# Kernel optimization log

Hardware: AMD Instinct MI355X
Metric: run time of the kernel (lower is better)

## Reference

```python
import jax, jax.numpy as jnp
import numpy as np

B, T, IN, H = 1024, 128, 5, 100  # batch, seq_len, input_size, hidden_size


def setup_inputs() -> dict:
    key = jax.random.key(0)
    ks = jax.random.split(key, 20)
    bound = 1.0 / np.sqrt(H)  # PyTorch LSTM init: U(-1/sqrt(H), 1/sqrt(H))

    def u(k, shape):
        return jax.random.uniform(k, shape, jnp.float32, -bound, bound)

    inp = {"x": jax.random.normal(ks[0], (B, T, IN), jnp.float32)}
    i = 1
    for layer, din in [(0, IN), (1, 2 * H)]:
        for d in ("f", "b"):
            inp[f"w_ih_l{layer}{d}"] = u(ks[i], (4 * H, din)); i += 1
            inp[f"w_hh_l{layer}{d}"] = u(ks[i], (4 * H, H)); i += 1
            inp[f"b_ih_l{layer}{d}"] = u(ks[i], (4 * H,)); i += 1
            inp[f"b_hh_l{layer}{d}"] = u(ks[i], (4 * H,)); i += 1
    inp["fc_w"] = u(ks[17], (3, 2 * H))
    inp["fc_b"] = u(ks[18], (3,))
    return inp


def _run_dir(x, w_ih, w_hh, b_ih, b_hh, reverse):
    """One LSTM direction. x: [B,T,D] -> hidden seq [B,T,H]. PyTorch gate order i,f,g,o."""
    xT = jnp.swapaxes(x, 0, 1)  # [T,B,D]
    # precompute input contribution for all timesteps: [T,B,4H]
    xg = jnp.einsum('tbd,gd->tbg', xT, w_ih) + b_ih + b_hh

    def step(carry, g_in):
        h, c = carry
        g = g_in + h @ w_hh.T  # [B,4H]
        i, f, gg, o = jnp.split(g, 4, axis=-1)
        c = jax.nn.sigmoid(f) * c + jax.nn.sigmoid(i) * jnp.tanh(gg)
        h = jax.nn.sigmoid(o) * jnp.tanh(c)
        return (h, c), h

    b = x.shape[0]
    init = (jnp.zeros((b, H), x.dtype), jnp.zeros((b, H), x.dtype))
    _, hs = jax.lax.scan(step, init, xg, reverse=reverse)  # hs[t] aligned with time t
    return jnp.swapaxes(hs, 0, 1)  # [B,T,H]


def reference(x,
              w_ih_l0f, w_hh_l0f, b_ih_l0f, b_hh_l0f,
              w_ih_l0b, w_hh_l0b, b_ih_l0b, b_hh_l0b,
              w_ih_l1f, w_hh_l1f, b_ih_l1f, b_hh_l1f,
              w_ih_l1b, w_hh_l1b, b_ih_l1b, b_hh_l1b,
              fc_w, fc_b):
    # Layer 0 (bidirectional): [B,T,2H]
    h0 = jnp.concatenate([
        _run_dir(x, w_ih_l0f, w_hh_l0f, b_ih_l0f, b_hh_l0f, False),
        _run_dir(x, w_ih_l0b, w_hh_l0b, b_ih_l0b, b_hh_l0b, True),
    ], axis=-1)
    # (inter-layer dropout p=0.2 is identity in eval mode)
    # Layer 1 (bidirectional): [B,T,2H]
    h1 = jnp.concatenate([
        _run_dir(h0, w_ih_l1f, w_hh_l1f, b_ih_l1f, b_hh_l1f, False),
        _run_dir(h0, w_ih_l1b, w_hh_l1b, b_ih_l1b, b_hh_l1b, True),
    ], axis=-1)
    last = h1[:, -1, :]  # [B,2H]
    # (dropout p=0.5 is identity in eval mode)
    logits = last @ fc_w.T + fc_b  # [B,3]
    return jax.nn.softmax(logits, axis=1)
```

## Files before the change

### kernel.cpp

```cpp
#include <hip/hip_runtime.h>
#include <hip/hip_fp16.h>


typedef __attribute__((ext_vector_type(8))) short bf16x8;
typedef __attribute__((ext_vector_type(4))) float f32x4;

constexpr int Bsz = 1024, Tt = 128, IN_ = 5, H = 100, G = 400, D1 = 200;
constexpr int NP = 512;
constexpr int NT = 25;
constexpr int MB = 8;

__device__ __forceinline__ float sigm(float x)   { return 1.f / (1.f + __expf(-x)); }
__device__ __forceinline__ float tanhf_(float x) { return 1.f - 2.f / (__expf(2.f * x) + 1.f); }
__device__ __forceinline__ unsigned short f2bf(float f) {
  unsigned u = __float_as_uint(f);
  u += 0x7fff + ((u >> 16) & 1);
  return (unsigned short)(u >> 16);
}
__device__ __forceinline__ float partner8(float v) {
  return __uint_as_float(
      (unsigned)__builtin_amdgcn_ds_swizzle((int)__float_as_uint(v), 0x17));
}

__device__ __forceinline__ void pack_body(
    const float* wA, int KA, const float* wB, int KB, int kbo,
    const float* b1, const float* b2, int bias_k,
    unsigned short* dst, int Kg, int idx) {
  if (idx >= Kg * NP * 8) return;
  int jj = idx & 7, rest = idx >> 3;
  int np_ = rest % NP, g = rest / NP;
  int j = np_ >> 2, gate = np_ & 3;
  int k = g * 8 + jj;
  float v = 0.f;
  if (j < H) {
    int n = gate * H + j;
    if (k < KA) v = wA[n * KA + k];
    else if (KB > 0 && k >= kbo && k < kbo + KB) v = wB[n * KB + (k - kbo)];
    else if (k == bias_k) v = b1[n] + b2[n];
  }
  dst[idx] = f2bf(v);
}

__global__ void pack_all(
    const float* __restrict__ w_hh_l0f, const float* __restrict__ w_ih_l0f,
    const float* __restrict__ b_ih_l0f, const float* __restrict__ b_hh_l0f,
    const float* __restrict__ w_hh_l0b, const float* __restrict__ w_ih_l0b,
    const float* __restrict__ b_ih_l0b, const float* __restrict__ b_hh_l0b,
    const float* __restrict__ w_hh_l1f, const float* __restrict__ b_ih_l1f,
    const float* __restrict__ b_hh_l1f,
    const float* __restrict__ w_ih_l1f, const float* __restrict__ w_ih_l1b,
    const float* __restrict__ b_ih_l1b, const float* __restrict__ b_hh_l1b,
    unsigned short* __restrict__ pk0f, unsigned short* __restrict__ pk0b,
    unsigned short* __restrict__ pkhh, unsigned short* __restrict__ pkxg,
    unsigned short* __restrict__ pk1b) {
  int idx = blockIdx.x * 256 + threadIdx.x;
  switch (blockIdx.y) {
    case 0: pack_body(w_hh_l0f, 100, w_ih_l0f, 5, 100, b_ih_l0f, b_hh_l0f, 105, pk0f, 16, idx); break;
    case 1: pack_body(w_hh_l0b, 100, w_ih_l0b, 5, 100, b_ih_l0b, b_hh_l0b, 105, pk0b, 16, idx); break;
    case 2: pack_body(w_hh_l1f, 100, nullptr, 0, 0, b_ih_l1f, b_hh_l1f, -1, pkhh, 16, idx); break;
    case 3: pack_body(w_ih_l1f, 200, nullptr, 0, 0, b_ih_l1f, b_hh_l1f, 200, pkxg, 28, idx); break;
    default: pack_body(w_ih_l1b, 200, nullptr, 0, 0, b_ih_l1b, b_hh_l1b, 200, pk1b, 28, idx);
  }
}

__global__ __launch_bounds__(1024, 1) void lstm_l0(
    const float* __restrict__ x,
    const unsigned short* __restrict__ pk_f, const unsigned short* __restrict__ pk_b,
    unsigned short* __restrict__ h0fT, unsigned short* __restrict__ h0bT) {
  __shared__ __align__(16) short A_s[2][16][16][8];

  const int tid = threadIdx.x;
  const int lane = tid & 63, w = tid >> 6;
  const int q = lane >> 4, l16 = lane & 15;
  const int b0 = blockIdx.x * MB;
  const int dir = blockIdx.y;
  const unsigned short* pk = dir ? pk_b : pk_f;
  unsigned short* hT = dir ? h0bT : h0fT;

  for (int i = tid; i < 2 * 16 * 16 * 8; i += 1024) ((short*)A_s)[i] = 0;

  const int mtA = w, mtB = w + 16;
  const bool bvalid = (mtB < NT);
  bf16x8 wfA[4], wfB[4];
#pragma unroll
  for (int kt = 0; kt < 4; ++kt) {
    wfA[kt] = *(const bf16x8*)(pk + ((size_t)(kt * 4 + q) * NP + mtA * 16 + l16) * 8);
    wfB[kt] = *(const bf16x8*)(pk + ((size_t)(kt * 4 + q) * NP + mtB * 16 + l16) * 8);
  }
  float c = 0.f;
  const bool up = (l16 >= 8);
  const int mm = l16 & 7;
  const int j = (up ? mtB : mtA) * 4 + q;
  const bool valid = up ? bvalid : true;
  const int xm = tid / IN_, xe = tid - xm * IN_;
  const int sm = tid / 25, sj = (tid - (tid / 25) * 25) * 4;
  const float* xp = x + ((size_t)(b0 + xm) * Tt + (dir ? Tt - 2 : 1)) * IN_ + xe;
  const int xstride = dir ? -IN_ : IN_;
  unsigned short* hp =
      hT + ((size_t)(dir ? Tt - 1 : 0) * Bsz + b0 + sm) * H + sj;
  const int hstride = dir ? -(Bsz * H) : (Bsz * H);
  __syncthreads();
  if (tid < 16) {
    A_s[0][13][tid][1] = (short)f2bf(1.f);
    A_s[1][13][tid][1] = (short)f2bf(1.f);
  }
  if (tid < MB * IN_) {
    int t0 = dir ? (Tt - 1) : 0;
    int k = 100 + xe;
    A_s[0][k >> 3][xm][k & 7] =
        (short)f2bf(x[((size_t)(b0 + xm) * Tt + t0) * IN_ + xe]);
  }
  __syncthreads();

  int p = 0;
  for (int step = 0; step < Tt; ++step) {
    if (step > 0 && tid < 200) {
      uint2 hv = *(const uint2*)&A_s[p][sj >> 3][sm][sj & 7];
      *(uint2*)hp = hv;
      hp += hstride;
    }
    float xn = 0.f;
    const bool do_x = (tid < MB * IN_) && (step < Tt - 1);
    if (do_x) { xn = *xp; xp += xstride; }
    bf16x8 hfrag[4];
#pragma unroll
    for (int kt = 0; kt < 4; ++kt) hfrag[kt] = *(const bf16x8*)A_s[p][kt * 4 + q][l16];
    f32x4 accA = (f32x4){0.f, 0.f, 0.f, 0.f};
    f32x4 accB = (f32x4){0.f, 0.f, 0.f, 0.f};
#pragma unroll
    for (int kt = 0; kt < 4; ++kt)
      accA = __builtin_amdgcn_mfma_f32_16x16x32_bf16(wfA[kt], hfrag[kt], accA, 0, 0, 0);
    if (bvalid) {
#pragma unroll
      for (int kt = 0; kt < 4; ++kt)
        accB = __builtin_amdgcn_mfma_f32_16x16x32_bf16(wfB[kt], hfrag[kt], accB, 0, 0, 0);
    }
    float pb0 = partner8(accB[0]), pb1 = partner8(accB[1]);
    float pb2 = partner8(accB[2]), pb3 = partner8(accB[3]);
    float g0 = up ? pb0 : accA[0];
    float g1 = up ? pb1 : accA[1];
    float g2 = up ? pb2 : accA[2];
    float g3 = up ? pb3 : accA[3];
    float cc = sigm(g1) * c + sigm(g0) * tanhf_(g2);
    c = cc;
    float h = sigm(g3) * tanhf_(cc);
    if (valid) A_s[1 - p][j >> 3][mm][j & 7] = (short)f2bf(h);
    if (do_x) {
      int k = 100 + xe;
      A_s[1 - p][k >> 3][xm][k & 7] = (short)f2bf(xn);
    }
    __syncthreads();
    p ^= 1;
  }
  if (tid < 200) *(uint2*)hp = *(const uint2*)&A_s[p][sj >> 3][sm][sj & 7];
}

__global__ __launch_bounds__(1024, 1) void gemm_xg(
    const unsigned short* __restrict__ h0fT, const unsigned short* __restrict__ h0bT,
    const unsigned short* __restrict__ pkw, __half* __restrict__ xg) {
  __shared__ __align__(16) short B_s[28][64][8];
  const int tid = threadIdx.x;
  const int lane = tid & 63, w = tid >> 6;
  const int q = lane >> 4, l16 = lane & 15;
  const int r0 = blockIdx.x * 64;
  const size_t base = (size_t)r0 * H;

  for (int i = tid; i < 3 * 64 * 8; i += 1024) {
    int jj = i & 7, gl = i >> 9;
    ((short*)&B_s[25][0][0])[i] = (short)((gl == 0 && jj == 0) ? f2bf(1.f) : 0);
  }
  for (int idx = tid; idx < 1600; idx += 1024) {
    int m = idx / 25, j0 = (idx - (idx / 25) * 25) * 4;
    *(uint2*)&B_s[j0 >> 3][m][j0 & 7] = *(const uint2*)(h0fT + base + m * H + j0);
    int k = 100 + j0;
    *(uint2*)&B_s[k >> 3][m][k & 7] = *(const uint2*)(h0bT + base + m * H + j0);
  }

  const int mtA = w, mtB = w + 16;
  const bool bvalid = (mtB < NT);
  bf16x8 wfA[7], wfB[7];
#pragma unroll
  for (int kt = 0; kt < 7; ++kt) {
    wfA[kt] = *(const bf16x8*)(pkw + ((size_t)(kt * 4 + q) * NP + mtA * 16 + l16) * 8);
    wfB[kt] = *(const bf16x8*)(pkw + ((size_t)(kt * 4 + q) * NP + mtB * 16 + l16) * 8);
  }
  const int jA = mtA * 4 + q, jB = mtB * 4 + q;
  __syncthreads();

#pragma unroll
  for (int rg = 0; rg < 4; ++rg) {
    f32x4 accA = (f32x4){0.f, 0.f, 0.f, 0.f};
    f32x4 accB = (f32x4){0.f, 0.f, 0.f, 0.f};
#pragma unroll
    for (int kt = 0; kt < 7; ++kt) {
      bf16x8 hf = *(const bf16x8*)B_s[kt * 4 + q][rg * 16 + l16];
      accA = __builtin_amdgcn_mfma_f32_16x16x32_bf16(wfA[kt], hf, accA, 0, 0, 0);
      if (bvalid)
        accB = __builtin_amdgcn_mfma_f32_16x16x32_bf16(wfB[kt], hf, accB, 0, 0, 0);
    }
    const size_t row = (size_t)(r0 + rg * 16 + l16);
    {
      __half2 h01 = __floats2half2_rn(accA[0], accA[1]);
      __half2 h23 = __floats2half2_rn(accA[2], accA[3]);
      uint2 st; *(__half2*)&st.x = h01; *(__half2*)&st.y = h23;
      *(uint2*)(xg + row * G + 4 * jA) = st;
    }
    if (bvalid) {
      __half2 h01 = __floats2half2_rn(accB[0], accB[1]);
      __half2 h23 = __floats2half2_rn(accB[2], accB[3]);
      uint2 st; *(__half2*)&st.x = h01; *(__half2*)&st.y = h23;
      *(uint2*)(xg + row * G + 4 * jB) = st;
    }
  }
}

__global__ __launch_bounds__(1024, 1) void lstm_l1(
    const unsigned short* __restrict__ h0fT, const unsigned short* __restrict__ h0bT,
    const unsigned short* __restrict__ pk_hh, const unsigned short* __restrict__ pk1b,
    const __half* __restrict__ xg,
    const float* __restrict__ fc_w, const float* __restrict__ fc_b,
    float* __restrict__ out) {
  __shared__ __align__(16) short A_s[2][16][16][8];
  __shared__ __align__(16) short A2_s[28][16][8];
  __shared__ float hf_s[MB][H];
  __shared__ float hb_s[MB][H];
  __shared__ float fcw_s[3 * D1];
  __shared__ float fcb_s[3];
  __shared__ float logit_s[MB][3];

  const int tid = threadIdx.x;
  const int lane = tid & 63, w = tid >> 6;
  const int q = lane >> 4, l16 = lane & 15;
  const int b0 = blockIdx.x * MB;
  const uint2* xg2 = (const uint2*)xg;

  for (int i = tid; i < 2 * 16 * 16 * 8; i += 1024) ((short*)A_s)[i] = 0;
  for (int i = tid; i < 25 * 16 * 8; i += 1024) ((short*)A2_s)[i] = 0;
  for (int i = tid; i < 3 * 16 * 8; i += 1024) {
    int jj = i & 7, gl = i >> 7;
    ((short*)&A2_s[25][0][0])[i] = (short)((gl == 0 && jj == 0) ? f2bf(1.f) : 0);
  }
  for (int i = tid; i < 3 * D1; i += 1024) fcw_s[i] = fc_w[i];
  if (tid < 3) fcb_s[tid] = fc_b[tid];

  const int mtA = w, mtB = w + 16;
  const bool bvalid = (mtB < NT);
  bf16x8 wfA[4], wfB[4];
#pragma unroll
  for (int kt = 0; kt < 4; ++kt) {
    wfA[kt] = *(const bf16x8*)(pk_hh + ((size_t)(kt * 4 + q) * NP + mtA * 16 + l16) * 8);
    wfB[kt] = *(const bf16x8*)(pk_hh + ((size_t)(kt * 4 + q) * NP + mtB * 16 + l16) * 8);
  }
  float c = 0.f;
  const bool up = (l16 >= 8);
  const int mm = l16 & 7;
  const int j = (up ? mtB : mtA) * 4 + q;
  const bool valid = up ? bvalid : true;
  const int jA = mtA * 4 + q;
  const int jB = mtB * 4 + q;
  const uint2* xgpA = xg2 + (size_t)(b0 + mm) * 100 + jA;
  const uint2* xgpB = xg2 + (size_t)(b0 + mm) * 100 + jB;
  uint2 xgCurA = xgpA[0], xgCurB = xgpB[0];
  xgpA += Bsz * 100; xgpB += Bsz * 100;
  __syncthreads();

  int p = 0;
  for (int t = 0; t < Tt; ++t) {
    uint2 xgNxtA = xgCurA, xgNxtB = xgCurB;
    if (t < Tt - 1) {
      xgNxtA = *xgpA; xgNxtB = *xgpB;
      xgpA += Bsz * 100; xgpB += Bsz * 100;
    }
    float2 a01 = __half22float2(*(const __half2*)&xgCurA.x);
    float2 a23 = __half22float2(*(const __half2*)&xgCurA.y);
    float2 b01 = __half22float2(*(const __half2*)&xgCurB.x);
    float2 b23 = __half22float2(*(const __half2*)&xgCurB.y);
    f32x4 accA = (f32x4){a01.x, a01.y, a23.x, a23.y};
    f32x4 accB = (f32x4){b01.x, b01.y, b23.x, b23.y};
    bf16x8 hfrag[4];
#pragma unroll
    for (int kt = 0; kt < 4; ++kt) hfrag[kt] = *(const bf16x8*)A_s[p][kt * 4 + q][l16];
#pragma unroll
    for (int kt = 0; kt < 4; ++kt)
      accA = __builtin_amdgcn_mfma_f32_16x16x32_bf16(wfA[kt], hfrag[kt], accA, 0, 0, 0);
    if (bvalid) {
#pragma unroll
      for (int kt = 0; kt < 4; ++kt)
        accB = __builtin_amdgcn_mfma_f32_16x16x32_bf16(wfB[kt], hfrag[kt], accB, 0, 0, 0);
    }
    float pb0 = partner8(accB[0]), pb1 = partner8(accB[1]);
    float pb2 = partner8(accB[2]), pb3 = partner8(accB[3]);
    float g0 = up ? pb0 : accA[0];
    float g1 = up ? pb1 : accA[1];
    float g2 = up ? pb2 : accA[2];
    float g3 = up ? pb3 : accA[3];
    float cc = sigm(g1) * c + sigm(g0) * tanhf_(g2);
    c = cc;
    float h = sigm(g3) * tanhf_(cc);
    if (valid) {
      A_s[1 - p][j >> 3][mm][j & 7] = (short)f2bf(h);
      if (t == Tt - 1) hf_s[mm][j] = h;
    }
    xgCurA = xgNxtA; xgCurB = xgNxtB;
    __syncthreads();
    p ^= 1;
  }

  {
    const size_t base = ((size_t)(Tt - 1) * Bsz + b0) * H;
    if (tid < 200) {
      int m = tid / 25, j0 = (tid - (tid / 25) * 25) * 4;
      *(uint2*)&A2_s[j0 >> 3][m][j0 & 7] = *(const uint2*)(h0fT + base + m * H + j0);
      int k = 100 + j0;
      *(uint2*)&A2_s[k >> 3][m][k & 7] = *(const uint2*)(h0bT + base + m * H + j0);
    }
  }
  __syncthreads();
  {
    f32x4 accA = (f32x4){0.f, 0.f, 0.f, 0.f};
    f32x4 accB = (f32x4){0.f, 0.f, 0.f, 0.f};
#pragma unroll
    for (int kt = 0; kt < 7; ++kt) {
      bf16x8 hf = *(const bf16x8*)A2_s[kt * 4 + q][l16];
      bf16x8 wfa = *(const bf16x8*)(pk1b + ((size_t)(kt * 4 + q) * NP + mtA * 16 + l16) * 8);
      accA = __builtin_amdgcn_mfma_f32_16x16x32_bf16(wfa, hf, accA, 0, 0, 0);
      if (bvalid) {
        bf16x8 wfb = *(const bf16x8*)(pk1b + ((size_t)(kt * 4 + q) * NP + mtB * 16 + l16) * 8);
        accB = __builtin_amdgcn_mfma_f32_16x16x32_bf16(wfb, hf, accB, 0, 0, 0);
      }
    }
    float pb0 = partner8(accB[0]);
    float pb2 = partner8(accB[2]);
    float pb3 = partner8(accB[3]);
    float g0 = up ? pb0 : accA[0];
    float g2 = up ? pb2 : accA[2];
    float g3 = up ? pb3 : accA[3];
    float cc = sigm(g0) * tanhf_(g2);
    if (valid) hb_s[mm][j] = sigm(g3) * tanhf_(cc);
  }
  __syncthreads();

  if (tid < MB * 3) {
    int m = tid / 3, cls = tid - m * 3;
    float s = fcb_s[cls];
    for (int jj = 0; jj < H; ++jj) s += fcw_s[cls * D1 + jj] * hf_s[m][jj];
    for (int jj = 0; jj < H; ++jj) s += fcw_s[cls * D1 + H + jj] * hb_s[m][jj];
    logit_s[m][cls] = s;
  }
  __syncthreads();
  if (tid < MB) {
    float a = logit_s[tid][0], b = logit_s[tid][1], cc = logit_s[tid][2];
    float mx = fmaxf(a, fmaxf(b, cc));
    float e0 = __expf(a - mx), e1 = __expf(b - mx), e2 = __expf(cc - mx);
    float inv = 1.f / (e0 + e1 + e2);
    out[(b0 + tid) * 3 + 0] = e0 * inv;
    out[(b0 + tid) * 3 + 1] = e1 * inv;
    out[(b0 + tid) * 3 + 2] = e2 * inv;
  }
}

extern "C" void kernel_launch(void* const* d_in, const int* in_sizes, int n_in,
                              void* d_out, int out_size, void* d_ws, size_t ws_size,
                              hipStream_t stream) {
  const float* x        = (const float*)d_in[0];
  const float* w_ih_l0f = (const float*)d_in[1];
  const float* w_hh_l0f = (const float*)d_in[2];
  const float* b_ih_l0f = (const float*)d_in[3];
  const float* b_hh_l0f = (const float*)d_in[4];
  const float* w_ih_l0b = (const float*)d_in[5];
  const float* w_hh_l0b = (const float*)d_in[6];
  const float* b_ih_l0b = (const float*)d_in[7];
  const float* b_hh_l0b = (const float*)d_in[8];
  const float* w_ih_l1f = (const float*)d_in[9];
  const float* w_hh_l1f = (const float*)d_in[10];
  const float* b_ih_l1f = (const float*)d_in[11];
  const float* b_hh_l1f = (const float*)d_in[12];
  const float* w_ih_l1b = (const float*)d_in[13];
  const float* b_ih_l1b = (const float*)d_in[15];
  const float* b_hh_l1b = (const float*)d_in[16];
  const float* fc_w     = (const float*)d_in[17];
  const float* fc_b     = (const float*)d_in[18];

  unsigned short* h0fT = (unsigned short*)d_ws;
  unsigned short* h0bT = h0fT + (size_t)Tt * Bsz * H;
  __half* xgT          = (__half*)(h0bT + (size_t)Tt * Bsz * H);
  unsigned short* pk0f = (unsigned short*)(xgT + (size_t)Tt * Bsz * G);
  unsigned short* pk0b = pk0f + 16 * NP * 8;
  unsigned short* pkhh = pk0b + 16 * NP * 8;
  unsigned short* pkxg = pkhh + 16 * NP * 8;
  unsigned short* pk1b = pkxg + 28 * NP * 8;

  pack_all<<<dim3(448, 5), 256, 0, stream>>>(
      w_hh_l0f, w_ih_l0f, b_ih_l0f, b_hh_l0f,
      w_hh_l0b, w_ih_l0b, b_ih_l0b, b_hh_l0b,
      w_hh_l1f, b_ih_l1f, b_hh_l1f,
      w_ih_l1f, w_ih_l1b, b_ih_l1b, b_hh_l1b,
      pk0f, pk0b, pkhh, pkxg, pk1b);

  lstm_l0<<<dim3(Bsz / MB, 2), 1024, 0, stream>>>(x, pk0f, pk0b, h0fT, h0bT);
  gemm_xg<<<(Bsz * Tt) / 64, 1024, 0, stream>>>(h0fT, h0bT, pkxg, xgT);
  lstm_l1<<<Bsz / MB, 1024, 0, stream>>>(h0fT, h0bT, pkhh, pk1b, xgT,
                                         fc_w, fc_b, (float*)d_out);
}
```

Baseline: 390.6 us.

## Halve layer-1 batch per block and regroup gate tiles across fewer waves

The layer-1 recurrent kernel now handles 4 batch rows per block instead of 8, so twice as many blocks (256) run to fill more CUs. Within a block only 7 waves do work, each owning 4 gate tiles. Each lane picks its gate values out of the four accumulators with a 4-lane swizzle. The MFMA tiles are now only a quarter used (4 of 16 columns), and each active wave does more serial MFMAs per timestep. That trades per-step latency for broader parallelism across CUs.

```diff
diff --git a/kernel.cpp b/kernel.cpp
--- a/kernel.cpp
+++ b/kernel.cpp
@@ -9,6 +9,7 @@
 constexpr int NP = 512;
 constexpr int NT = 25;
 constexpr int MB = 8;
+constexpr int MB1 = 4;
 
 __device__ __forceinline__ float sigm(float x)   { return 1.f / (1.f + __expf(-x)); }
 __device__ __forceinline__ float tanhf_(float x) { return 1.f - 2.f / (__expf(2.f * x) + 1.f); }
@@ -20,6 +21,10 @@
 __device__ __forceinline__ float partner8(float v) {
   return __uint_as_float(
       (unsigned)__builtin_amdgcn_ds_swizzle((int)__float_as_uint(v), 0x17));
+}
+__device__ __forceinline__ float partner4(float v) {
+  return __uint_as_float(
+      (unsigned)__builtin_amdgcn_ds_swizzle((int)__float_as_uint(v), 0x13));
 }
 
 __device__ __forceinline__ void pack_body(
@@ -222,16 +227,16 @@
     float* __restrict__ out) {
   __shared__ __align__(16) short A_s[2][16][16][8];
   __shared__ __align__(16) short A2_s[28][16][8];
-  __shared__ float hf_s[MB][H];
-  __shared__ float hb_s[MB][H];
+  __shared__ float hf_s[MB1][H];
+  __shared__ float hb_s[MB1][H];
   __shared__ float fcw_s[3 * D1];
   __shared__ float fcb_s[3];
-  __shared__ float logit_s[MB][3];
+  __shared__ float logit_s[MB1][3];
 
   const int tid = threadIdx.x;
   const int lane = tid & 63, w = tid >> 6;
   const int q = lane >> 4, l16 = lane & 15;
-  const int b0 = blockIdx.x * MB;
+  const int b0 = blockIdx.x * MB1;
   const uint2* xg2 = (const uint2*)xg;
 
   for (int i = tid; i < 2 * 16 * 16 * 8; i += 1024) ((short*)A_s)[i] = 0;
@@ -243,112 +248,121 @@
   for (int i = tid; i < 3 * D1; i += 1024) fcw_s[i] = fc_w[i];
   if (tid < 3) fcb_s[tid] = fc_b[tid];
 
-  const int mtA = w, mtB = w + 16;
-  const bool bvalid = (mtB < NT);
-  bf16x8 wfA[4], wfB[4];
-#pragma unroll
-  for (int kt = 0; kt < 4; ++kt) {
-    wfA[kt] = *(const bf16x8*)(pk_hh + ((size_t)(kt * 4 + q) * NP + mtA * 16 + l16) * 8);
-    wfB[kt] = *(const bf16x8*)(pk_hh + ((size_t)(kt * 4 + q) * NP + mtB * 16 + l16) * 8);
+  const bool busy = (w < 7);
+  const int m = l16 & 3, g16 = l16 >> 2;
+  const int myMt = w * 4 + g16;
+  const int jme = myMt * 4 + q;
+  const bool evalid = busy && (myMt < NT);
+  int mts[4]; bool tv[4];
+  bf16x8 wf[4][4];
+  if (busy) {
+#pragma unroll
+    for (int i = 0; i < 4; ++i) {
+      int mt = w * 4 + i; mts[i] = mt; tv[i] = (mt < NT);
+#pragma unroll
+      for (int kt = 0; kt < 4; ++kt)
+        wf[i][kt] = *(const bf16x8*)(pk_hh + ((size_t)(kt * 4 + q) * NP + mt * 16 + l16) * 8);
+    }
   }
   float c = 0.f;
-  const bool up = (l16 >= 8);
-  const int mm = l16 & 7;
-  const int j = (up ? mtB : mtA) * 4 + q;
-  const bool valid = up ? bvalid : true;
-  const int jA = mtA * 4 + q;
-  const int jB = mtB * 4 + q;
-  const uint2* xgpA = xg2 + (size_t)(b0 + mm) * 100 + jA;
-  const uint2* xgpB = xg2 + (size_t)(b0 + mm) * 100 + jB;
-  uint2 xgCurA = xgpA[0], xgCurB = xgpB[0];
-  xgpA += Bsz * 100; xgpB += Bsz * 100;
+  const uint2* xgp = xg2 + (size_t)(b0 + m) * 100 + jme;
+  uint2 xgCur = {0, 0};
+  if (busy) { xgCur = *xgp; xgp += Bsz * 100; }
   __syncthreads();
 
   int p = 0;
   for (int t = 0; t < Tt; ++t) {
-    uint2 xgNxtA = xgCurA, xgNxtB = xgCurB;
-    if (t < Tt - 1) {
-      xgNxtA = *xgpA; xgNxtB = *xgpB;
-      xgpA += Bsz * 100; xgpB += Bsz * 100;
-    }
-    float2 a01 = __half22float2(*(const __half2*)&xgCurA.x);
-    float2 a23 = __half22float2(*(const __half2*)&xgCurA.y);
-    float2 b01 = __half22float2(*(const __half2*)&xgCurB.x);
-    float2 b23 = __half22float2(*(const __half2*)&xgCurB.y);
-    f32x4 accA = (f32x4){a01.x, a01.y, a23.x, a23.y};
-    f32x4 accB = (f32x4){b01.x, b01.y, b23.x, b23.y};
-    bf16x8 hfrag[4];
-#pragma unroll
-    for (int kt = 0; kt < 4; ++kt) hfrag[kt] = *(const bf16x8*)A_s[p][kt * 4 + q][l16];
-#pragma unroll
-    for (int kt = 0; kt < 4; ++kt)
-      accA = __builtin_amdgcn_mfma_f32_16x16x32_bf16(wfA[kt], hfrag[kt], accA, 0, 0, 0);
-    if (bvalid) {
-#pragma unroll
-      for (int kt = 0; kt < 4; ++kt)
-        accB = __builtin_amdgcn_mfma_f32_16x16x32_bf16(wfB[kt], hfrag[kt], accB, 0, 0, 0);
-    }
-    float pb0 = partner8(accB[0]), pb1 = partner8(accB[1]);
-    float pb2 = partner8(accB[2]), pb3 = partner8(accB[3]);
-    float g0 = up ? pb0 : accA[0];
-    float g1 = up ? pb1 : accA[1];
-    float g2 = up ? pb2 : accA[2];
-    float g3 = up ? pb3 : accA[3];
-    float cc = sigm(g1) * c + sigm(g0) * tanhf_(g2);
-    c = cc;
-    float h = sigm(g3) * tanhf_(cc);
-    if (valid) {
-      A_s[1 - p][j >> 3][mm][j & 7] = (short)f2bf(h);
-      if (t == Tt - 1) hf_s[mm][j] = h;
-    }
-    xgCurA = xgNxtA; xgCurB = xgNxtB;
+    if (busy) {
+      uint2 xgNxt = xgCur;
+      if (t < Tt - 1) { xgNxt = *xgp; xgp += Bsz * 100; }
+      bf16x8 hfrag[4];
+#pragma unroll
+      for (int kt = 0; kt < 4; ++kt) hfrag[kt] = *(const bf16x8*)A_s[p][kt * 4 + q][l16];
+      f32x4 acc[4];
+#pragma unroll
+      for (int i = 0; i < 4; ++i) {
+        acc[i] = (f32x4){0.f, 0.f, 0.f, 0.f};
+        if (!tv[i]) continue;
+#pragma unroll
+        for (int kt = 0; kt < 4; ++kt)
+          acc[i] = __builtin_amdgcn_mfma_f32_16x16x32_bf16(wf[i][kt], hfrag[kt], acc[i], 0, 0, 0);
+      }
+      float2 x01 = __half22float2(*(const __half2*)&xgCur.x);
+      float2 x23 = __half22float2(*(const __half2*)&xgCur.y);
+      float xr[4] = {x01.x, x01.y, x23.x, x23.y};
+      float gr[4];
+#pragma unroll
+      for (int r = 0; r < 4; ++r) {
+        float v0 = partner4(acc[0][r]);
+        float v1 = partner4(acc[1][r]);
+        float v2 = partner4(acc[2][r]);
+        float v3 = partner4(acc[3][r]);
+        float lo = (g16 & 1) ? v1 : v0;
+        float hi = (g16 & 1) ? v3 : v2;
+        gr[r] = ((g16 & 2) ? hi : lo) + xr[r];
+      }
+      float cc = sigm(gr[1]) * c + sigm(gr[0]) * tanhf_(gr[2]);
+      c = cc;
+      float h = sigm(gr[3]) * tanhf_(cc);
+      if (evalid) {
+        A_s[1 - p][jme >> 3][m][jme & 7] = (short)f2bf(h);
+        if (t == Tt - 1) hf_s[m][jme] = h;
+      }
+      xgCur = xgNxt;
+    }
     __syncthreads();
     p ^= 1;
   }
 
   {
     const size_t base = ((size_t)(Tt - 1) * Bsz + b0) * H;
-    if (tid < 200) {
-      int m = tid / 25, j0 = (tid - (tid / 25) * 25) * 4;
-      *(uint2*)&A2_s[j0 >> 3][m][j0 & 7] = *(const uint2*)(h0fT + base + m * H + j0);
+    if (tid < 100) {
+      int m2 = tid / 25, j0 = (tid - (tid / 25) * 25) * 4;
+      *(uint2*)&A2_s[j0 >> 3][m2][j0 & 7] = *(const uint2*)(h0fT + base + m2 * H + j0);
       int k = 100 + j0;
-      *(uint2*)&A2_s[k >> 3][m][k & 7] = *(const uint2*)(h0bT + base + m * H + j0);
-    }
-  }
-  __syncthreads();
-  {
-    f32x4 accA = (f32x4){0.f, 0.f, 0.f, 0.f};
-    f32x4 accB = (f32x4){0.f, 0.f, 0.f, 0.f};
+      *(uint2*)&A2_s[k >> 3][m2][k & 7] = *(const uint2*)(h0bT + base + m2 * H + j0);
+    }
+  }
+  __syncthreads();
+  if (busy) {
+    f32x4 acc[4];
+#pragma unroll
+    for (int i = 0; i < 4; ++i) acc[i] = (f32x4){0.f, 0.f, 0.f, 0.f};
 #pragma unroll
     for (int kt = 0; kt < 7; ++kt) {
       bf16x8 hf = *(const bf16x8*)A2_s[kt * 4 + q][l16];
-      bf16x8 wfa = *(const bf16x8*)(pk1b + ((size_t)(kt * 4 + q) * NP + mtA * 16 + l16) * 8);
-      accA = __builtin_amdgcn_mfma_f32_16x16x32_bf16(wfa, hf, accA, 0, 0, 0);
-      if (bvalid) {
-        bf16x8 wfb = *(const bf16x8*)(pk1b + ((size_t)(kt * 4 + q) * NP + mtB * 16 + l16) * 8);
-        accB = __builtin_amdgcn_mfma_f32_16x16x32_bf16(wfb, hf, accB, 0, 0, 0);
+#pragma unroll
+      for (int i = 0; i < 4; ++i) {
+        if (!tv[i]) continue;
+        bf16x8 wfb = *(const bf16x8*)(pk1b + ((size_t)(kt * 4 + q) * NP + mts[i] * 16 + l16) * 8);
+        acc[i] = __builtin_amdgcn_mfma_f32_16x16x32_bf16(wfb, hf, acc[i], 0, 0, 0);
       }
     }
-    float pb0 = partner8(accB[0]);
-    float pb2 = partner8(accB[2]);
-    float pb3 = partner8(accB[3]);
-    float g0 = up ? pb0 : accA[0];
-    float g2 = up ? pb2 : accA[2];
-    float g3 = up ? pb3 : accA[3];
-    float cc = sigm(g0) * tanhf_(g2);
-    if (valid) hb_s[mm][j] = sigm(g3) * tanhf_(cc);
-  }
-  __syncthreads();
-
-  if (tid < MB * 3) {
-    int m = tid / 3, cls = tid - m * 3;
+    float gr[4];
+#pragma unroll
+    for (int r = 0; r < 4; ++r) {
+      float v0 = partner4(acc[0][r]);
+      float v1 = partner4(acc[1][r]);
+      float v2 = partner4(acc[2][r]);
+      float v3 = partner4(acc[3][r]);
+      float lo = (g16 & 1) ? v1 : v0;
+      float hi = (g16 & 1) ? v3 : v2;
+      gr[r] = (g16 & 2) ? hi : lo;
+    }
+    float cc = sigm(gr[0]) * tanhf_(gr[2]);
+    if (evalid) hb_s[m][jme] = sigm(gr[3]) * tanhf_(cc);
+  }
+  __syncthreads();
+
+  if (tid < MB1 * 3) {
+    int mr = tid / 3, cls = tid - mr * 3;
     float s = fcb_s[cls];
-    for (int jj = 0; jj < H; ++jj) s += fcw_s[cls * D1 + jj] * hf_s[m][jj];
-    for (int jj = 0; jj < H; ++jj) s += fcw_s[cls * D1 + H + jj] * hb_s[m][jj];
-    logit_s[m][cls] = s;
-  }
-  __syncthreads();
-  if (tid < MB) {
+    for (int jj = 0; jj < H; ++jj) s += fcw_s[cls * D1 + jj] * hf_s[mr][jj];
+    for (int jj = 0; jj < H; ++jj) s += fcw_s[cls * D1 + H + jj] * hb_s[mr][jj];
+    logit_s[mr][cls] = s;
+  }
+  __syncthreads();
+  if (tid < MB1) {
     float a = logit_s[tid][0], b = logit_s[tid][1], cc = logit_s[tid][2];
     float mx = fmaxf(a, fmaxf(b, cc));
     float e0 = __expf(a - mx), e1 = __expf(b - mx), e2 = __expf(cc - mx);
@@ -399,6 +413,6 @@
 
   lstm_l0<<<dim3(Bsz / MB, 2), 1024, 0, stream>>>(x, pk0f, pk0b, h0fT, h0bT);
   gemm_xg<<<(Bsz * Tt) / 64, 1024, 0, stream>>>(h0fT, h0bT, pkxg, xgT);
-  lstm_l1<<<Bsz / MB, 1024, 0, stream>>>(h0fT, h0bT, pkhh, pk1b, xgT,
-                                         fc_w, fc_b, (float*)d_out);
-}
+  lstm_l1<<<Bsz / MB1, 1024, 0, stream>>>(h0fT, h0bT, pkhh, pk1b, xgT,
+                                          fc_w, fc_b, (float*)d_out);
+}
```

New measurement: 376.2 us, median of 2. 3.7% less time.
